# Kernel optimization log

Measured on AMD Instinct MI355X. Metric: run time of the kernel, lower is better.

The kernel has to match this reference:

```python
import jax, jax.numpy as jnp
import numpy as np

P, S, C, F, B = 2, 2, 64, 64, 64


def setup_inputs() -> dict:
    key = jax.random.key(0)
    kx, kq, kw = jax.random.split(key, 3)
    X = jax.random.normal(kx, (B, P * S * C * F), dtype=jnp.float32)
    # sparse connection-strength tensor, densified; nonnegative small values
    dbfc = jax.random.uniform(kq, (P, S, C, F, C, F), dtype=jnp.float32) * 0.01
    wV = jax.random.normal(kw, (F, F), dtype=jnp.float32) * (1.0 / np.sqrt(F))
    return {"X": X, "databaseFeatureConnections": dbfc, "wV": wV}


def reference(X, databaseFeatureConnections, wV):
    p, s, c, f = (databaseFeatureConnections.shape[0], databaseFeatureConnections.shape[1],
                  databaseFeatureConnections.shape[2], databaseFeatureConnections.shape[3])
    b = X.shape[0]
    # wV: nn.Linear(f, f, bias=False) -> x @ W.T
    v = (X.reshape(b, p * s * c, f) @ wV.T).reshape(b, p, s, c, f)
    # kqHead.sum(dim=1).sum(dim=2): collapse both feature axes -> [p, s, c, c]
    scores = databaseFeatureConnections.sum(axis=(3, 5))
    weights = jax.nn.softmax(scores, axis=-1)  # [p, s, c, c]
    # per-head bmm: weights[p,s] @ v[:,p,s] -> [b, c, f] per head; heads concatenated
    # along feature dim in (p outer, s inner) order == reshape of [b, c, p, s, f]
    out = jnp.einsum('pscd,bpsdf->bcpsf', weights, v).reshape(b, c, p * s * f)
    # permute(1, 0, 2) -> [c, b, p*s*f]
    return out.transpose(1, 0, 2)
```

## Files before the change

kernel.cpp:

```cpp
#include <hip/hip_runtime.h>
#include <math.h>


typedef float floatx4 __attribute__((ext_vector_type(4)));

__global__ __launch_bounds__(256) void scores_partial_kernel(
    const float* __restrict__ dbfc, float* __restrict__ partials)
{
    const int bid   = blockIdx.x;
    const int slab  = bid >> 2;
    const int chunk = bid & 3;
    const int t     = threadIdx.x;

    const floatx4* src = reinterpret_cast<const floatx4*>(dbfc)
                       + (size_t)bid * 16384 + 2 * t;

    floatx4 e0 = (floatx4)0.f, e1 = (floatx4)0.f;
    floatx4 o0 = (floatx4)0.f, o1 = (floatx4)0.f;
#pragma unroll 4
    for (int i = 0; i < 32; ++i) {
        floatx4 v0 = __builtin_nontemporal_load(&src[i * 512 + 0]);
        floatx4 v1 = __builtin_nontemporal_load(&src[i * 512 + 1]);
        if (i & 1) { o0 += v0; o1 += v1; }
        else       { e0 += v0; e1 += v1; }
    }
    floatx4 es = e0 + e1, os = o0 + o1;
    float se = (es.x + es.y) + (es.z + es.w);
    float so = (os.x + os.y) + (os.z + os.w);
#pragma unroll
    for (int m = 1; m < 8; m <<= 1) {
        se += __shfl_xor(se, m, 64);
        so += __shfl_xor(so, m, 64);
    }
    if ((t & 7) == 0) {
        float* dst = partials + (size_t)chunk * 16384 + slab * 64;
        dst[(t >> 3)]      = se;
        dst[(t >> 3) + 32] = so;
    }
}

__global__ __launch_bounds__(256) void attn_out_kernel(
    const float* __restrict__ X, const float* __restrict__ wV,
    const float* __restrict__ partials, float* __restrict__ out)
{
    const int blk = blockIdx.x;
    const int ps  = blk >> 6;
    const int b   = blk & 63;
    const int t   = threadIdx.x;
    const int tc  = t >> 4;
    const int tf  = t & 15;

    __shared__ float Xs [64][68];
    __shared__ float wVs[64][68];
    __shared__ float Ws [64][68];
    __shared__ float VsT[64][68];

    const float4* xsrc = reinterpret_cast<const float4*>(X + (size_t)b * 16384 + ps * 4096);
    const float4* wsrc = reinterpret_cast<const float4*>(wV);
    const float4* psrc = reinterpret_cast<const float4*>(partials);
#pragma unroll
    for (int idx = t; idx < 1024; idx += 256) {
        int r = idx >> 4, jq = idx & 15, j = jq * 4;
        *reinterpret_cast<float4*>(&Xs [r][j]) = xsrc[idx];
        *reinterpret_cast<float4*>(&wVs[r][j]) = wsrc[idx];
        float4 s = make_float4(0.f, 0.f, 0.f, 0.f);
#pragma unroll
        for (int k = 0; k < 4; ++k) {
            float4 p = psrc[k * 4096 + (ps * 64 + r) * 16 + jq];
            s.x += p.x; s.y += p.y; s.z += p.z; s.w += p.w;
        }
        *reinterpret_cast<float4*>(&Ws [r][j]) = s;
    }
    __syncthreads();

    float acc[4][4] = {};
    for (int f0 = 0; f0 < 64; f0 += 4) {
        float4 xa[4], wv[4];
#pragma unroll
        for (int ci = 0; ci < 4; ++ci)
            xa[ci] = *reinterpret_cast<const float4*>(&Xs[4 * tc + ci][f0]);
#pragma unroll
        for (int fi = 0; fi < 4; ++fi)
            wv[fi] = *reinterpret_cast<const float4*>(&wVs[tf + 16 * fi][f0]);
#pragma unroll
        for (int ci = 0; ci < 4; ++ci)
#pragma unroll
            for (int fi = 0; fi < 4; ++fi)
                acc[ci][fi] += xa[ci].x * wv[fi].x + xa[ci].y * wv[fi].y
                             + xa[ci].z * wv[fi].z + xa[ci].w * wv[fi].w;
    }

    {
        const int row = t >> 2, q = (t & 3) * 16;
        float e[16];
        float mx = -INFINITY;
#pragma unroll
        for (int i = 0; i < 16; ++i) mx = fmaxf(mx, Ws[row][q + i]);
        mx = fmaxf(mx, __shfl_xor(mx, 1, 64));
        mx = fmaxf(mx, __shfl_xor(mx, 2, 64));
        float sum = 0.f;
#pragma unroll
        for (int i = 0; i < 16; ++i) { e[i] = expf(Ws[row][q + i] - mx); sum += e[i]; }
        sum += __shfl_xor(sum, 1, 64);
        sum += __shfl_xor(sum, 2, 64);
        const float rinv = 1.0f / sum;
#pragma unroll
        for (int i = 0; i < 16; ++i) Ws[row][q + i] = e[i] * rinv;
    }

#pragma unroll
    for (int ci = 0; ci < 4; ++ci)
#pragma unroll
        for (int fi = 0; fi < 4; ++fi)
            VsT[tf + 16 * fi][4 * tc + ci] = acc[ci][fi];
    __syncthreads();

    float o[4][4] = {};
    for (int d = 0; d < 64; d += 4) {
        float4 wa[4], va[4];
#pragma unroll
        for (int ci = 0; ci < 4; ++ci)
            wa[ci] = *reinterpret_cast<const float4*>(&Ws[4 * tc + ci][d]);
#pragma unroll
        for (int fi = 0; fi < 4; ++fi)
            va[fi] = *reinterpret_cast<const float4*>(&VsT[tf + 16 * fi][d]);
#pragma unroll
        for (int ci = 0; ci < 4; ++ci)
#pragma unroll
            for (int fi = 0; fi < 4; ++fi)
                o[ci][fi] += wa[ci].x * va[fi].x + wa[ci].y * va[fi].y
                           + wa[ci].z * va[fi].z + wa[ci].w * va[fi].w;
    }

#pragma unroll
    for (int ci = 0; ci < 4; ++ci) {
        const int c = 4 * tc + ci;
        float* orow = out + ((size_t)c * 64 + b) * 256 + ps * 64;
#pragma unroll
        for (int fi = 0; fi < 4; ++fi)
            orow[tf + 16 * fi] = o[ci][fi];
    }
}

extern "C" void kernel_launch(void* const* d_in, const int* in_sizes, int n_in,
                              void* d_out, int out_size, void* d_ws, size_t ws_size,
                              hipStream_t stream)
{
    const float* X    = (const float*)d_in[0];
    const float* dbfc = (const float*)d_in[1];
    const float* wV   = (const float*)d_in[2];
    float* out        = (float*)d_out;
    float* partials   = (float*)d_ws;

    scores_partial_kernel<<<1024, 256, 0, stream>>>(dbfc, partials);
    attn_out_kernel<<<256, 256, 0, stream>>>(X, wV, partials, out);
}
```

Baseline: 59.49 us.

## Split score reduction into 2048 blocks with per-wave shuffle and LDS combine

The dbfc reduction kernel now uses twice as many blocks, each summing half as much data (8 chunks per slab instead of 4). Each wave loads 16-lane-contiguous floatx4 rows, does a horizontal sum, reduces across 16 lanes with shuffles, and combines the 4 waves through shared memory, so each block writes 64 contiguous outputs. The aim is more memory-level parallelism and occupancy on the dominant 64MB streaming read. The cost is more shuffle work per thread, an extra barrier, and twice as many partials for the attention kernel to sum.

```diff
diff --git a/kernel.cpp b/kernel.cpp
--- a/kernel.cpp
+++ b/kernel.cpp
@@ -4,38 +4,49 @@
 
 typedef float floatx4 __attribute__((ext_vector_type(4)));
 
-__global__ __launch_bounds__(256) void scores_partial_kernel(
+__global__ __launch_bounds__(256, 8) void scores_partial_kernel(
     const float* __restrict__ dbfc, float* __restrict__ partials)
 {
     const int bid   = blockIdx.x;
-    const int slab  = bid >> 2;
-    const int chunk = bid & 3;
+    const int slab  = bid >> 3;
+    const int chunk = bid & 7;
     const int t     = threadIdx.x;
+    const int w     = t >> 6;
+    const int l     = t & 63;
+    const int g     = l >> 4;
 
     const floatx4* src = reinterpret_cast<const floatx4*>(dbfc)
-                       + (size_t)bid * 16384 + 2 * t;
+                       + (size_t)bid * 8192 + w * 2048 + l;
 
-    floatx4 e0 = (floatx4)0.f, e1 = (floatx4)0.f;
-    floatx4 o0 = (floatx4)0.f, o1 = (floatx4)0.f;
-#pragma unroll 4
-    for (int i = 0; i < 32; ++i) {
-        floatx4 v0 = __builtin_nontemporal_load(&src[i * 512 + 0]);
-        floatx4 v1 = __builtin_nontemporal_load(&src[i * 512 + 1]);
-        if (i & 1) { o0 += v0; o1 += v1; }
-        else       { e0 += v0; e1 += v1; }
+    float acc[16];
+#pragma unroll
+    for (int k = 0; k < 16; ++k) acc[k] = 0.f;
+
+#pragma unroll
+    for (int k = 0; k < 16; ++k) {
+        floatx4 a = __builtin_nontemporal_load(&src[k * 64]);
+        floatx4 b = __builtin_nontemporal_load(&src[(k + 16) * 64]);
+        acc[k] += ((a.x + a.y) + (a.z + a.w)) + ((b.x + b.y) + (b.z + b.w));
     }
-    floatx4 es = e0 + e1, os = o0 + o1;
-    float se = (es.x + es.y) + (es.z + es.w);
-    float so = (os.x + os.y) + (os.z + os.w);
+
 #pragma unroll
-    for (int m = 1; m < 8; m <<= 1) {
-        se += __shfl_xor(se, m, 64);
-        so += __shfl_xor(so, m, 64);
+    for (int k = 0; k < 16; ++k) {
+#pragma unroll
+        for (int m = 1; m < 16; m <<= 1)
+            acc[k] += __shfl_xor(acc[k], m, 64);
     }
-    if ((t & 7) == 0) {
-        float* dst = partials + (size_t)chunk * 16384 + slab * 64;
-        dst[(t >> 3)]      = se;
-        dst[(t >> 3) + 32] = so;
+    float myv = 0.f;
+#pragma unroll
+    for (int k = 0; k < 16; ++k)
+        if ((l & 15) == k) myv = acc[k];
+
+    __shared__ float sm[4][64];
+    sm[w][4 * (l & 15) + g] = myv;
+    __syncthreads();
+
+    if (t < 64) {
+        float s = sm[0][t] + sm[1][t] + sm[2][t] + sm[3][t];
+        partials[(size_t)chunk * 16384 + slab * 64 + t] = s;
     }
 }
 
@@ -65,7 +76,7 @@
         *reinterpret_cast<float4*>(&wVs[r][j]) = wsrc[idx];
         float4 s = make_float4(0.f, 0.f, 0.f, 0.f);
 #pragma unroll
-        for (int k = 0; k < 4; ++k) {
+        for (int k = 0; k < 8; ++k) {
             float4 p = psrc[k * 4096 + (ps * 64 + r) * 16 + jq];
             s.x += p.x; s.y += p.y; s.z += p.z; s.w += p.w;
         }
@@ -152,6 +163,6 @@
     float* out        = (float*)d_out;
     float* partials   = (float*)d_ws;
 
-    scores_partial_kernel<<<1024, 256, 0, stream>>>(dbfc, partials);
+    scores_partial_kernel<<<2048, 256, 0, stream>>>(dbfc, partials);
     attn_out_kernel<<<256, 256, 0, stream>>>(X, wV, partials, out);
 }
```

Measured after the change: 66.96 us. +12.6%, slower.
